# Performance work log

Measured on AMD Instinct MI355X. Metric: run time of the kernel, lower is better.

The kernel has to match this reference:

```python
import jax, jax.numpy as jnp
import numpy as np

N = 50000
E = 800000
IN_DIM = 128
HID = 64
OUT_DIM = 1
NEG_SLOPE = 0.2
EPS = 1e-16


def _glorot(key, shape):
    fan = shape[-1] + (shape[0] if len(shape) > 1 else shape[-1])
    lim = jnp.sqrt(6.0 / fan)
    return jax.random.uniform(key, shape, jnp.float32, -lim, lim)


def setup_inputs() -> dict:
    key = jax.random.key(0)
    ks = jax.random.split(key, 12)
    x = jax.random.normal(ks[0], (N, IN_DIM), jnp.float32)
    edge_index = jax.random.randint(ks[1], (2, E), 0, N, jnp.int64)
    # GATConv layer 1: in=128, out=64, heads=4, concat=True
    W1 = _glorot(ks[2], (4 * HID, IN_DIM))
    att_src1 = _glorot(ks[3], (4, HID))
    att_dst1 = _glorot(ks[4], (4, HID))
    b1 = jnp.zeros((4 * HID,), jnp.float32)
    # GATConv layer 2: in=256, out=64, heads=1, concat=True
    W2 = _glorot(ks[5], (HID, 4 * HID))
    att_src2 = _glorot(ks[6], (1, HID))
    att_dst2 = _glorot(ks[7], (1, HID))
    b2 = jnp.zeros((HID,), jnp.float32)
    # final Linear(hidden, 1)
    fc_w = _glorot(ks[8], (OUT_DIM, HID))
    fc_b = jnp.zeros((OUT_DIM,), jnp.float32)
    return {"x": x, "edge_index": edge_index, "W1": W1, "att_src1": att_src1,
            "att_dst1": att_dst1, "b1": b1, "W2": W2, "att_src2": att_src2,
            "att_dst2": att_dst2, "b2": b2, "fc_w": fc_w, "fc_b": fc_b}


def _gat_layer(x, src, dst, W, att_src, att_dst, bias, heads, out_ch):
    n = x.shape[0]
    xt = (x @ W.T).reshape(n, heads, out_ch)          # [N, H, C]
    a_src = jnp.sum(xt * att_src[None], axis=-1)      # [N, H]
    a_dst = jnp.sum(xt * att_dst[None], axis=-1)      # [N, H]
    e = a_src[src] + a_dst[dst]                       # [E', H]
    e = jnp.where(e > 0, e, NEG_SLOPE * e)            # LeakyReLU(0.2)
    # segment softmax over incoming edges of each dst node
    m = jax.ops.segment_max(e, dst, num_segments=n)
    e = jnp.exp(e - m[dst])
    s = jax.ops.segment_sum(e, dst, num_segments=n)
    alpha = e / (s[dst] + EPS)                        # [E', H]
    msg = xt[src] * alpha[:, :, None]                 # [E', H, C]
    out = jax.ops.segment_sum(msg, dst, num_segments=n)
    return out.reshape(n, heads * out_ch) + bias


def reference(x, edge_index, W1, att_src1, att_dst1, b1,
              W2, att_src2, att_dst2, b2, fc_w, fc_b):
    n = x.shape[0]
    # PyG GATConv default: add self-loops
    loops = jnp.arange(n, dtype=edge_index.dtype)
    src = jnp.concatenate([edge_index[0], loops])
    dst = jnp.concatenate([edge_index[1], loops])
    h = jax.nn.relu(_gat_layer(x, src, dst, W1, att_src1, att_dst1, b1, 4, HID))
    h = jax.nn.relu(_gat_layer(h, src, dst, W2, att_src2, att_dst2, b2, 1, HID))
    logits = h @ fc_w.T + fc_b                        # [N, 1]
    return jax.nn.sigmoid(logits).squeeze()
```

## Files before the change

### kernel.cpp

```cpp
#include <hip/hip_runtime.h>
#include <hip/hip_bf16.h>

#define NN 50000
#define EE 800000
#define ET (NN + EE)
#define SG ((NN + 255) / 256)
#define GB1 ((NN + 63) / 64)
#define GA  391
#define GBB (GB1 - GA)
#define HB  782

typedef __attribute__((ext_vector_type(8))) short short8;
typedef __attribute__((ext_vector_type(4))) short short4b;
typedef __attribute__((ext_vector_type(4))) float f32x4;

__device__ __forceinline__ float bf2f(unsigned short u) {
    union { unsigned int i; float f; } v; v.i = ((unsigned int)u) << 16; return v.f;
}
__device__ __forceinline__ unsigned short f2bf(float f) {
    __hip_bfloat16 h = __float2bfloat16(f);
    return *reinterpret_cast<unsigned short*>(&h);
}
__device__ __forceinline__ float lrelu(float e) { return fmaxf(e, 0.2f * e); }


__global__ __launch_bounds__(256) void k_scan1(const int* __restrict__ cnt,
                                               int* __restrict__ tmp, int* __restrict__ bsum) {
    int b = blockIdx.x, t = threadIdx.x, i = b * 256 + t;
    int lane = t & 63, w = t >> 6;
    int v = (i < NN) ? cnt[i] : 0;
    int s = v;
    #pragma unroll
    for (int off = 1; off < 64; off <<= 1) {
        int u = __shfl_up(s, off);
        if (lane >= off) s += u;
    }
    __shared__ int ws[4];
    if (lane == 63) ws[w] = s;
    __syncthreads();
    if (t == 0) {
        int a = 0;
        #pragma unroll
        for (int k = 0; k < 4; k++) { int x = ws[k]; ws[k] = a; a += x; }
        bsum[b] = a;
    }
    __syncthreads();
    s += ws[w];
    if (i < NN) tmp[i] = s;
}

__global__ __launch_bounds__(256) void k_scan2(const int* __restrict__ bsum, int* __restrict__ boff) {
    int t = threadIdx.x, lane = t & 63, w = t >> 6;
    int v = (t < SG) ? bsum[t] : 0;
    int s = v;
    #pragma unroll
    for (int off = 1; off < 64; off <<= 1) {
        int u = __shfl_up(s, off);
        if (lane >= off) s += u;
    }
    __shared__ int ws[4];
    if (lane == 63) ws[w] = s;
    __syncthreads();
    if (t == 0) {
        int a = 0;
        #pragma unroll
        for (int k = 0; k < 4; k++) { int x = ws[k]; ws[k] = a; a += x; }
    }
    __syncthreads();
    s += ws[w];
    if (t < SG) boff[t] = s - v;
}

__global__ void k_scan3_prep(const int* __restrict__ tmp, const int* __restrict__ boff,
                             int* __restrict__ rowptr, int* __restrict__ csr) {
    int i = blockIdx.x * blockDim.x + threadIdx.x;
    if (i == 0) rowptr[0] = 0;
    if (i < NN) {
        int base = boff[i >> 8];
        int incl = tmp[i] + base + i + 1;
        rowptr[i + 1] = incl;
        int excl = ((i & 255) ? tmp[i - 1] + base : base) + i;
        csr[excl] = i;
    }
}

template<int K, int N, int NH, bool A_BF16, bool B_BF16>
__device__ __forceinline__ void gemm_body(
    int bid, const void* __restrict__ Aptr, const void* __restrict__ Wptr,
    const float* __restrict__ atts, const float* __restrict__ attd,
    unsigned short* __restrict__ C, float* __restrict__ as_, float* __restrict__ ad_,
    int M)
{
    constexpr int KU  = K / 8;
    constexpr int KUH = KU / 2;
    constexpr int KC  = K / 32;
    constexpr int NW  = N / 4;
    constexpr int NI  = NW / 16;
    constexpr int ABYTES = 64 * KU * 16;
    constexpr int BBYTES = N * KUH * 16;
    constexpr int SMEM = ABYTES + BBYTES + (NH == 1 ? 2048 : 0);
    __shared__ char smem[SMEM];
    char* Ash = smem;
    char* Bsh = smem + ABYTES;
    unsigned short* Csh = (unsigned short*)smem;
    float* scsh = (float*)(smem + ABYTES + BBYTES);

    int t = threadIdx.x;
    int lane = t & 63, w = t >> 6;
    int colL = lane & 15, quad = lane >> 4;
    int m0 = bid * 64;

    {
        constexpr int CNT = 64 * KU / 256;
        #pragma unroll
        for (int i = 0; i < CNT; i++) {
            int v = t + 256 * i;
            int m = v / KU, u = v % KU;
            int gr = m0 + m; if (gr >= M) gr = M - 1;
            short8 val;
            if (A_BF16) {
                val = *(const short8*)((const unsigned short*)Aptr + (size_t)gr * K + u * 8);
            } else {
                const float* Af = (const float*)Aptr;
                float4 lo = *(const float4*)(Af + (size_t)gr * K + u * 8);
                float4 hi = *(const float4*)(Af + (size_t)gr * K + u * 8 + 4);
                val[0] = (short)f2bf(lo.x); val[1] = (short)f2bf(lo.y);
                val[2] = (short)f2bf(lo.z); val[3] = (short)f2bf(lo.w);
                val[4] = (short)f2bf(hi.x); val[5] = (short)f2bf(hi.y);
                val[6] = (short)f2bf(hi.z); val[7] = (short)f2bf(hi.w);
            }
            *(short8*)(Ash + ((size_t)m * KU + (u ^ (m & 7))) * 16) = val;
        }
    }

    f32x4 acc[4][NI];
    #pragma unroll
    for (int mi = 0; mi < 4; mi++)
        #pragma unroll
        for (int ni = 0; ni < NI; ni++) acc[mi][ni] = (f32x4){0.f, 0.f, 0.f, 0.f};

    #pragma unroll
    for (int kh = 0; kh < 2; kh++) {
        __syncthreads();
        {
            constexpr int CNT = N * KUH / 256;
            #pragma unroll
            for (int i = 0; i < CNT; i++) {
                int v = t + 256 * i;
                int n = v / KUH, uu = v % KUH;
                int u = kh * KUH + uu;
                short8 val;
                if (B_BF16) {
                    val = *(const short8*)((const unsigned short*)Wptr + (size_t)n * K + u * 8);
                } else {
                    const float* Wf = (const float*)Wptr;
                    float4 lo = *(const float4*)(Wf + (size_t)n * K + u * 8);
                    float4 hi = *(const float4*)(Wf + (size_t)n * K + u * 8 + 4);
                    val[0] = (short)f2bf(lo.x); val[1] = (short)f2bf(lo.y);
                    val[2] = (short)f2bf(lo.z); val[3] = (short)f2bf(lo.w);
                    val[4] = (short)f2bf(hi.x); val[5] = (short)f2bf(hi.y);
                    val[6] = (short)f2bf(hi.z); val[7] = (short)f2bf(hi.w);
                }
                *(short8*)(Bsh + ((size_t)n * KUH + (uu ^ (n & 7))) * 16) = val;
            }
        }
        __syncthreads();
        #pragma unroll
        for (int kcl = 0; kcl < KC / 2; kcl++) {
            int uA = (kh * (KC / 2) + kcl) * 4 + quad;
            int uB = kcl * 4 + quad;
            short8 bfr[NI];
            #pragma unroll
            for (int ni = 0; ni < NI; ni++) {
                int n = w * NW + ni * 16 + colL;
                bfr[ni] = *(const short8*)(Bsh + ((size_t)n * KUH + (uB ^ (n & 7))) * 16);
            }
            #pragma unroll
            for (int mi = 0; mi < 4; mi++) {
                int m = mi * 16 + colL;
                short8 af = *(const short8*)(Ash + ((size_t)m * KU + (uA ^ (m & 7))) * 16);
                #pragma unroll
                for (int ni = 0; ni < NI; ni++)
                    acc[mi][ni] = __builtin_amdgcn_mfma_f32_16x16x32_bf16(af, bfr[ni], acc[mi][ni], 0, 0, 0);
            }
        }
    }
    __syncthreads();

    float asv[NI], adv[NI];
    #pragma unroll
    for (int ni = 0; ni < NI; ni++) {
        int na = (NH == 4) ? (w * 64 + ni * 16 + colL) : (w * 16 + colL);
        asv[ni] = atts[na];
        adv[ni] = attd[na];
    }
    #pragma unroll
    for (int mi = 0; mi < 4; mi++) {
        float ps[4] = {0.f, 0.f, 0.f, 0.f}, pd[4] = {0.f, 0.f, 0.f, 0.f};
        #pragma unroll
        for (int ni = 0; ni < NI; ni++)
            #pragma unroll
            for (int r = 0; r < 4; r++) {
                ps[r] += acc[mi][ni][r] * asv[ni];
                pd[r] += acc[mi][ni][r] * adv[ni];
            }
        #pragma unroll
        for (int off = 1; off < 16; off <<= 1)
            #pragma unroll
            for (int r = 0; r < 4; r++) {
                ps[r] += __shfl_xor(ps[r], off);
                pd[r] += __shfl_xor(pd[r], off);
            }
        if (colL == 0) {
            #pragma unroll
            for (int r = 0; r < 4; r++) {
                int rloc = mi * 16 + quad * 4 + r;
                if (NH == 4) {
                    int row = m0 + rloc;
                    if (row < M) {
                        as_[(size_t)row * 4 + w] = ps[r];
                        ad_[(size_t)row * 4 + w] = pd[r];
                    }
                } else {
                    scsh[(w * 64 + rloc) * 2 + 0] = ps[r];
                    scsh[(w * 64 + rloc) * 2 + 1] = pd[r];
                }
            }
        }
    }

    #pragma unroll
    for (int mi = 0; mi < 4; mi++)
        #pragma unroll
        for (int ni = 0; ni < NI; ni++)
            #pragma unroll
            for (int r = 0; r < 4; r++)
                Csh[(size_t)(mi * 16 + quad * 4 + r) * (N + 8) + w * NW + ni * 16 + colL] =
                    f2bf(acc[mi][ni][r]);
    __syncthreads();

    {
        constexpr int CNT = 64 * (N / 8) / 256;
        #pragma unroll
        for (int i = 0; i < CNT; i++) {
            int v = t + 256 * i;
            int m = v / (N / 8), u = v % (N / 8);
            int row = m0 + m;
            if (row < M)
                *(short8*)(C + (size_t)row * N + u * 8) =
                    *(const short8*)(Csh + (size_t)m * (N + 8) + u * 8);
        }
    }
    if (NH == 1 && t < 64) {
        int row = m0 + t;
        if (row < M) {
            float s = 0.f, d = 0.f;
            #pragma unroll
            for (int ww = 0; ww < 4; ww++) {
                s += scsh[(ww * 64 + t) * 2 + 0];
                d += scsh[(ww * 64 + t) * 2 + 1];
            }
            as_[row] = s;
            ad_[row] = d;
        }
    }
}

template<int K, int N, int NH, bool A_BF16, bool B_BF16>
__global__ __launch_bounds__(256) void k_gemm_mfma(
    const void* __restrict__ Aptr, const void* __restrict__ Wptr,
    const float* __restrict__ atts, const float* __restrict__ attd,
    unsigned short* __restrict__ C, float* __restrict__ as_, float* __restrict__ ad_,
    int M)
{
    gemm_body<K, N, NH, A_BF16, B_BF16>(blockIdx.x, Aptr, Wptr, atts, attd, C, as_, ad_, M);
}

__global__ __launch_bounds__(256) void k_gemm1_hist(
    const void* __restrict__ Aptr, const void* __restrict__ Wptr,
    const float* __restrict__ atts, const float* __restrict__ attd,
    unsigned short* __restrict__ C, float* __restrict__ as_, float* __restrict__ ad_,
    int M,
    const int* __restrict__ dst, int* __restrict__ cnt, int* __restrict__ rank,
    const float* __restrict__ W2, unsigned short* __restrict__ w2b)
{
    int bid = blockIdx.x;
    bool isg; int ord;
    if (bid < 2 * GA) { isg = !(bid & 1); ord = bid >> 1; }
    else              { isg = false;      ord = bid - GA; }
    if (isg) {
        gemm_body<128, 256, 4, false, false>(ord, Aptr, Wptr, atts, attd, C, as_, ad_, M);
    } else {
        int t = threadIdx.x;
        if (ord < 16) {
            int j = ord * 256 + t;
            float4 v = *(const float4*)(W2 + j * 4);
            short4b o;
            o[0] = (short)f2bf(v.x); o[1] = (short)f2bf(v.y);
            o[2] = (short)f2bf(v.z); o[3] = (short)f2bf(v.w);
            *(short4b*)(w2b + j * 4) = o;
        }
        int i4 = ord * 256 + t;
        if (i4 < EE / 4) {
            int base = i4 * 4;
            int4 d = *(const int4*)(dst + base);
            int4 rr;
            rr.x = atomicAdd(&cnt[d.x], 1);
            rr.y = atomicAdd(&cnt[d.y], 1);
            rr.z = atomicAdd(&cnt[d.z], 1);
            rr.w = atomicAdd(&cnt[d.w], 1);
            *(int4*)(rank + base) = rr;
        }
    }
}

__global__ __launch_bounds__(256) void k_gemm1_scatter(
    const void* __restrict__ Aptr, const void* __restrict__ Wptr,
    const float* __restrict__ atts, const float* __restrict__ attd,
    unsigned short* __restrict__ C, float* __restrict__ as_, float* __restrict__ ad_,
    int M,
    const int* __restrict__ src, const int* __restrict__ dst,
    const int* __restrict__ rank, const int* __restrict__ rowptr,
    int* __restrict__ csr)
{
    int bid = blockIdx.x;
    bool isg; int ord;
    if (bid < 2 * GBB) { isg = !(bid & 1); ord = bid >> 1; }
    else               { isg = false;      ord = bid - GBB; }
    if (isg) {
        gemm_body<128, 256, 4, false, false>(GA + ord, Aptr, Wptr, atts, attd, C, as_, ad_, M);
    } else {
        int i4 = ord * 256 + threadIdx.x;
        if (i4 < EE / 4) {
            int base = i4 * 4;
            int4 d = *(const int4*)(dst + base);
            int4 r = *(const int4*)(rank + base);
            int4 s = *(const int4*)(src + base);
            csr[rowptr[d.x] + 1 + r.x] = s.x;
            csr[rowptr[d.y] + 1 + r.y] = s.y;
            csr[rowptr[d.z] + 1 + r.z] = s.z;
            csr[rowptr[d.w] + 1 + r.w] = s.w;
        }
    }
}

__global__ __launch_bounds__(256) void k_l1_agg(
    const unsigned short* __restrict__ xt1, const float* __restrict__ as1,
    const float* __restrict__ ad1, const int* __restrict__ rowptr,
    const int* __restrict__ csr, const float* __restrict__ b1,
    unsigned short* __restrict__ h1)
{
    int t = threadIdx.x;
    int lane = t & 63, w = t >> 6;
    int n = blockIdx.x * 4 + w;
    int beg = rowptr[n], deg = rowptr[n + 1] - beg;
    int half = lane >> 5, c = lane & 31, h = c >> 3;
    float adh = ad1[n * 4 + h];
    const char* xb = (const char*)xt1;
    const char* ab = (const char*)as1;
    unsigned co = (unsigned)(c << 4);
    unsigned ho = (unsigned)(h << 2);

    float acc[8] = {0.f, 0.f, 0.f, 0.f, 0.f, 0.f, 0.f, 0.f};
    float esum = 0.f;
    int j = 0;
    for (; j + 8 <= deg; j += 8) {
        int p = beg + j + half * 4;
        int s0 = csr[p], s1 = csr[p + 1], s2 = csr[p + 2], s3 = csr[p + 3];
        float a0 = *(const float*)(ab + ((unsigned)(s0 << 4) + ho));
        float a1 = *(const float*)(ab + ((unsigned)(s1 << 4) + ho));
        float a2 = *(const float*)(ab + ((unsigned)(s2 << 4) + ho));
        float a3 = *(const float*)(ab + ((unsigned)(s3 << 4) + ho));
        short8 r0 = *(const short8*)(xb + ((unsigned)(s0 << 9) + co));
        short8 r1 = *(const short8*)(xb + ((unsigned)(s1 << 9) + co));
        short8 r2 = *(const short8*)(xb + ((unsigned)(s2 << 9) + co));
        short8 r3 = *(const short8*)(xb + ((unsigned)(s3 << 9) + co));
        float e0 = __expf(lrelu(a0 + adh));
        float e1 = __expf(lrelu(a1 + adh));
        float e2 = __expf(lrelu(a2 + adh));
        float e3 = __expf(lrelu(a3 + adh));
        esum += (e0 + e1) + (e2 + e3);
        #pragma unroll
        for (int k = 0; k < 8; k++)
            acc[k] += (bf2f((unsigned short)r0[k]) * e0 + bf2f((unsigned short)r1[k]) * e1)
                    + (bf2f((unsigned short)r2[k]) * e2 + bf2f((unsigned short)r3[k]) * e3);
    }
    if (j + 4 <= deg) {
        int p = beg + j + half * 2;
        int s0 = csr[p], s1 = csr[p + 1];
        float a0 = *(const float*)(ab + ((unsigned)(s0 << 4) + ho));
        float a1 = *(const float*)(ab + ((unsigned)(s1 << 4) + ho));
        short8 r0 = *(const short8*)(xb + ((unsigned)(s0 << 9) + co));
        short8 r1 = *(const short8*)(xb + ((unsigned)(s1 << 9) + co));
        float e0 = __expf(lrelu(a0 + adh));
        float e1 = __expf(lrelu(a1 + adh));
        esum += e0 + e1;
        #pragma unroll
        for (int k = 0; k < 8; k++)
            acc[k] += bf2f((unsigned short)r0[k]) * e0 + bf2f((unsigned short)r1[k]) * e1;
        j += 4;
    }
    for (; j < deg; j += 2) {
        int jj = j + half;
        if (jj < deg) {
            int s = csr[beg + jj];
            float a0 = *(const float*)(ab + ((unsigned)(s << 4) + ho));
            short8 r = *(const short8*)(xb + ((unsigned)(s << 9) + co));
            float e = __expf(lrelu(a0 + adh));
            esum += e;
            #pragma unroll
            for (int k = 0; k < 8; k++) acc[k] += bf2f((unsigned short)r[k]) * e;
        }
    }
    #pragma unroll
    for (int k = 0; k < 8; k++) acc[k] += __shfl_xor(acc[k], 32);
    esum += __shfl_xor(esum, 32);
    if (half == 0) {
        float rs = 1.f / (esum + 1e-16f);
        float4 bl = *(const float4*)(b1 + c * 8);
        float4 bh = *(const float4*)(b1 + c * 8 + 4);
        float bb[8] = {bl.x, bl.y, bl.z, bl.w, bh.x, bh.y, bh.z, bh.w};
        short8 o;
        #pragma unroll
        for (int k = 0; k < 8; k++)
            o[k] = (short)f2bf(fmaxf(acc[k] * rs + bb[k], 0.f));
        *(short8*)(h1 + (size_t)n * 256 + c * 8) = o;
    }
}

__global__ __launch_bounds__(256) void k_l2_agg(
    const unsigned short* __restrict__ xt2, const float* __restrict__ as2,
    const float* __restrict__ ad2, const int* __restrict__ rowptr,
    const int* __restrict__ csr, const float* __restrict__ b2,
    const float* __restrict__ fcw, const float* __restrict__ fcb,
    float* __restrict__ out)
{
    int t = threadIdx.x;
    int lane = t & 63, w = t >> 6;
    int n = blockIdx.x * 4 + w;
    int beg = rowptr[n], deg = rowptr[n + 1] - beg;
    int q = lane >> 4, c = lane & 15;
    float adv = ad2[n];
    const char* xb = (const char*)xt2;
    unsigned co = (unsigned)(c << 3);

    float acc[4] = {0.f, 0.f, 0.f, 0.f};
    float esum = 0.f;
    int j = 0;
    if (deg >= 16) {
        int p = beg + q * 4;
        int s0 = csr[p], s1 = csr[p + 1], s2 = csr[p + 2], s3 = csr[p + 3];
        float a0 = as2[s0], a1 = as2[s1], a2 = as2[s2], a3 = as2[s3];
        uint2 r0 = *(const uint2*)(xb + ((unsigned)(s0 << 7) + co));
        uint2 r1 = *(const uint2*)(xb + ((unsigned)(s1 << 7) + co));
        uint2 r2 = *(const uint2*)(xb + ((unsigned)(s2 << 7) + co));
        uint2 r3 = *(const uint2*)(xb + ((unsigned)(s3 << 7) + co));
        for (; j + 32 <= deg; j += 16) {
            int p2 = beg + j + 16 + q * 4;
            int u0 = csr[p2], u1 = csr[p2 + 1], u2 = csr[p2 + 2], u3 = csr[p2 + 3];
            float f0 = as2[u0], f1 = as2[u1], f2 = as2[u2], f3 = as2[u3];
            uint2 q0 = *(const uint2*)(xb + ((unsigned)(u0 << 7) + co));
            uint2 q1 = *(const uint2*)(xb + ((unsigned)(u1 << 7) + co));
            uint2 q2 = *(const uint2*)(xb + ((unsigned)(u2 << 7) + co));
            uint2 q3 = *(const uint2*)(xb + ((unsigned)(u3 << 7) + co));
            float e0 = __expf(lrelu(a0 + adv));
            float e1 = __expf(lrelu(a1 + adv));
            float e2 = __expf(lrelu(a2 + adv));
            float e3 = __expf(lrelu(a3 + adv));
            esum += (e0 + e1) + (e2 + e3);
            acc[0] += (bf2f((unsigned short)(r0.x & 0xffff)) * e0 + bf2f((unsigned short)(r1.x & 0xffff)) * e1)
                    + (bf2f((unsigned short)(r2.x & 0xffff)) * e2 + bf2f((unsigned short)(r3.x & 0xffff)) * e3);
            acc[1] += (bf2f((unsigned short)(r0.x >> 16)) * e0 + bf2f((unsigned short)(r1.x >> 16)) * e1)
                    + (bf2f((unsigned short)(r2.x >> 16)) * e2 + bf2f((unsigned short)(r3.x >> 16)) * e3);
            acc[2] += (bf2f((unsigned short)(r0.y & 0xffff)) * e0 + bf2f((unsigned short)(r1.y & 0xffff)) * e1)
                    + (bf2f((unsigned short)(r2.y & 0xffff)) * e2 + bf2f((unsigned short)(r3.y & 0xffff)) * e3);
            acc[3] += (bf2f((unsigned short)(r0.y >> 16)) * e0 + bf2f((unsigned short)(r1.y >> 16)) * e1)
                    + (bf2f((unsigned short)(r2.y >> 16)) * e2 + bf2f((unsigned short)(r3.y >> 16)) * e3);
            a0 = f0; a1 = f1; a2 = f2; a3 = f3;
            r0 = q0; r1 = q1; r2 = q2; r3 = q3;
        }
        {
            float e0 = __expf(lrelu(a0 + adv));
            float e1 = __expf(lrelu(a1 + adv));
            float e2 = __expf(lrelu(a2 + adv));
            float e3 = __expf(lrelu(a3 + adv));
            esum += (e0 + e1) + (e2 + e3);
            acc[0] += (bf2f((unsigned short)(r0.x & 0xffff)) * e0 + bf2f((unsigned short)(r1.x & 0xffff)) * e1)
                    + (bf2f((unsigned short)(r2.x & 0xffff)) * e2 + bf2f((unsigned short)(r3.x & 0xffff)) * e3);
            acc[1] += (bf2f((unsigned short)(r0.x >> 16)) * e0 + bf2f((unsigned short)(r1.x >> 16)) * e1)
                    + (bf2f((unsigned short)(r2.x >> 16)) * e2 + bf2f((unsigned short)(r3.x >> 16)) * e3);
            acc[2] += (bf2f((unsigned short)(r0.y & 0xffff)) * e0 + bf2f((unsigned short)(r1.y & 0xffff)) * e1)
                    + (bf2f((unsigned short)(r2.y & 0xffff)) * e2 + bf2f((unsigned short)(r3.y & 0xffff)) * e3);
            acc[3] += (bf2f((unsigned short)(r0.y >> 16)) * e0 + bf2f((unsigned short)(r1.y >> 16)) * e1)
                    + (bf2f((unsigned short)(r2.y >> 16)) * e2 + bf2f((unsigned short)(r3.y >> 16)) * e3);
            j += 16;
        }
    }
    if (j + 8 <= deg) {
        int p = beg + j + q * 2;
        int s0 = csr[p], s1 = csr[p + 1];
        float a0 = as2[s0], a1 = as2[s1];
        uint2 r0 = *(const uint2*)(xb + ((unsigned)(s0 << 7) + co));
        uint2 r1 = *(const uint2*)(xb + ((unsigned)(s1 << 7) + co));
        float e0 = __expf(lrelu(a0 + adv));
        float e1 = __expf(lrelu(a1 + adv));
        esum += e0 + e1;
        acc[0] += bf2f((unsigned short)(r0.x & 0xffff)) * e0 + bf2f((unsigned short)(r1.x & 0xffff)) * e1;
        acc[1] += bf2f((unsigned short)(r0.x >> 16)) * e0 + bf2f((unsigned short)(r1.x >> 16)) * e1;
        acc[2] += bf2f((unsigned short)(r0.y & 0xffff)) * e0 + bf2f((unsigned short)(r1.y & 0xffff)) * e1;
        acc[3] += bf2f((unsigned short)(r0.y >> 16)) * e0 + bf2f((unsigned short)(r1.y >> 16)) * e1;
        j += 8;
    }
    for (; j < deg; j += 4) {
        int jj = j + q;
        if (jj < deg) {
            int s = csr[beg + jj];
            float a0 = as2[s];
            uint2 r = *(const uint2*)(xb + ((unsigned)(s << 7) + co));
            float e = __expf(lrelu(a0 + adv));
            esum += e;
            acc[0] += bf2f((unsigned short)(r.x & 0xffff)) * e;
            acc[1] += bf2f((unsigned short)(r.x >> 16)) * e;
            acc[2] += bf2f((unsigned short)(r.y & 0xffff)) * e;
            acc[3] += bf2f((unsigned short)(r.y >> 16)) * e;
        }
    }
    #pragma unroll
    for (int k = 0; k < 4; k++) {
        acc[k] += __shfl_xor(acc[k], 16);
        acc[k] += __shfl_xor(acc[k], 32);
    }
    esum += __shfl_xor(esum, 16);
    esum += __shfl_xor(esum, 32);
    float rs = 1.f / (esum + 1e-16f);
    float4 bv = *(const float4*)(b2 + c * 4);
    float4 fv = *(const float4*)(fcw + c * 4);
    float z = fmaxf(acc[0] * rs + bv.x, 0.f) * fv.x
            + fmaxf(acc[1] * rs + bv.y, 0.f) * fv.y
            + fmaxf(acc[2] * rs + bv.z, 0.f) * fv.z
            + fmaxf(acc[3] * rs + bv.w, 0.f) * fv.w;
    #pragma unroll
    for (int off = 8; off; off >>= 1) z += __shfl_xor(z, off);
    if (lane == 0) out[n] = 1.f / (1.f + __expf(-(z + fcb[0])));
}


extern "C" void kernel_launch(void* const* d_in, const int* in_sizes, int n_in,
                              void* d_out, int out_size, void* d_ws, size_t ws_size,
                              hipStream_t stream) {
    const float* x    = (const float*)d_in[0];
    const int*   ei   = (const int*)d_in[1];
    const float* W1   = (const float*)d_in[2];
    const float* as1w = (const float*)d_in[3];
    const float* ad1w = (const float*)d_in[4];
    const float* b1   = (const float*)d_in[5];
    const float* W2   = (const float*)d_in[6];
    const float* as2w = (const float*)d_in[7];
    const float* ad2w = (const float*)d_in[8];
    const float* b2   = (const float*)d_in[9];
    const float* fcw  = (const float*)d_in[10];
    const float* fcb  = (const float*)d_in[11];
    float* out = (float*)d_out;

    const int* src = ei;
    const int* dst = ei + EE;

    char* base = (char*)d_ws;
    size_t off = 0;
    auto alloc = [&](size_t bytes) -> void* {
        void* p = base + off;
        off = (off + bytes + 255) & ~(size_t)255;
        return p;
    };
    int*   rowptr   = (int*)alloc((NN + 1) * sizeof(int));
    int*   cnt      = (int*)alloc(NN * sizeof(int));
    int*   tmp      = (int*)alloc(NN * sizeof(int));
    int*   bsum     = (int*)alloc(SG * sizeof(int));
    int*   boff     = (int*)alloc(SG * sizeof(int));
    int*   rank     = (int*)alloc(EE * sizeof(int));
    int*   csr      = (int*)alloc(ET * sizeof(int));
    unsigned short* xt1 = (unsigned short*)alloc((size_t)NN * 256 * sizeof(unsigned short));
    unsigned short* h1  = (unsigned short*)alloc((size_t)NN * 256 * sizeof(unsigned short));
    unsigned short* w2b = (unsigned short*)alloc(64 * 256 * sizeof(unsigned short));
    float* as1      = (float*)alloc(NN * 4 * sizeof(float));
    float* ad1      = (float*)alloc(NN * 4 * sizeof(float));
    float* as2      = (float*)alloc(NN * sizeof(float));
    float* ad2      = (float*)alloc(NN * sizeof(float));
    unsigned short* xt2 = xt1;

    hipMemsetAsync(cnt, 0, NN * sizeof(int), stream);

    k_gemm1_hist<<<2 * GA + (HB - GA), 256, 0, stream>>>(
        x, W1, as1w, ad1w, xt1, as1, ad1, NN, dst, cnt, rank, W2, w2b);

    k_scan1<<<SG, 256, 0, stream>>>(cnt, tmp, bsum);
    k_scan2<<<1, 256, 0, stream>>>(bsum, boff);
    k_scan3_prep<<<SG, 256, 0, stream>>>(tmp, boff, rowptr, csr);

    k_gemm1_scatter<<<2 * GBB + (HB - GBB), 256, 0, stream>>>(
        x, W1, as1w, ad1w, xt1, as1, ad1, NN, src, dst, rank, rowptr, csr);

    k_l1_agg<<<(NN + 3) / 4, 256, 0, stream>>>(xt1, as1, ad1, rowptr, csr, b1, h1);
    k_gemm_mfma<256, 64, 1, true, true><<<GB1, 256, 0, stream>>>(
        h1, w2b, as2w, ad2w, xt2, as2, ad2, NN);
    k_l2_agg<<<(NN + 3) / 4, 256, 0, stream>>>(xt2, as2, ad2, rowptr, csr, b2, fcw, fcb, out);
}
```

Before: 267.0 us.

## Fuse three-kernel scan into decoupled look-back scan; widen layer-2 aggregation loads

Replaces the three-pass prefix scan (block scan, block-sum scan, fixup) with a single-pass decoupled look-back scan. Each block publishes its aggregate or inclusive prefix through flagged atomics and spins on its predecessors. This saves two kernel launches and the intermediate tmp/boff round-trips. Separately, the layer-2 aggregation now has each lane load 16-byte rows covering 8 channels instead of 8-byte rows covering 4, with 8 edge groups per wavefront instead of 4. That adds one more shuffle reduction stage and relies on forward progress of earlier blocks for the spin-wait.

```diff
diff --git a/kernel.cpp b/kernel.cpp
--- a/kernel.cpp
+++ b/kernel.cpp
@@ -23,9 +23,10 @@
 }
 __device__ __forceinline__ float lrelu(float e) { return fmaxf(e, 0.2f * e); }
 
-
-__global__ __launch_bounds__(256) void k_scan1(const int* __restrict__ cnt,
-                                               int* __restrict__ tmp, int* __restrict__ bsum) {
+__global__ __launch_bounds__(256) void k_scan_fused(
+    const int* __restrict__ cnt, int* __restrict__ st,
+    int* __restrict__ rowptr, int* __restrict__ csr)
+{
     int b = blockIdx.x, t = threadIdx.x, i = b * 256 + t;
     int lane = t & 63, w = t >> 6;
     int v = (i < NN) ? cnt[i] : 0;
@@ -36,50 +37,54 @@
         if (lane >= off) s += u;
     }
     __shared__ int ws[4];
+    __shared__ int exsh;
     if (lane == 63) ws[w] = s;
     __syncthreads();
+    int a = 0;
     if (t == 0) {
-        int a = 0;
         #pragma unroll
         for (int k = 0; k < 4; k++) { int x = ws[k]; ws[k] = a; a += x; }
-        bsum[b] = a;
+        int flag = (b == 0) ? 2 : 1;
+        __hip_atomic_store(&st[b], (a << 2) | flag, __ATOMIC_RELEASE, __HIP_MEMORY_SCOPE_AGENT);
+    }
+    if (w == 0 && b > 0) {
+        int ex = 0;
+        int base = b - 1;
+        for (;;) {
+            int idx = base - lane;
+            int pv = 0;
+            if (idx >= 0) {
+                do {
+                    pv = __hip_atomic_load(&st[idx], __ATOMIC_ACQUIRE, __HIP_MEMORY_SCOPE_AGENT);
+                } while ((pv & 3) == 0);
+            }
+            bool incl = (idx >= 0) && ((pv & 3) == 2);
+            unsigned long long m = __ballot(incl);
+            int contrib;
+            if (m) {
+                int fi = __ffsll((long long)m) - 1;
+                contrib = (idx >= 0 && lane <= fi) ? (pv >> 2) : 0;
+            } else {
+                contrib = (idx >= 0) ? (pv >> 2) : 0;
+            }
+            #pragma unroll
+            for (int off = 1; off < 64; off <<= 1) contrib += __shfl_xor(contrib, off);
+            ex += contrib;
+            if (m) break;
+            base -= 64;
+        }
+        if (lane == 0) {
+            __hip_atomic_store(&st[b], ((a + ex) << 2) | 2, __ATOMIC_RELEASE, __HIP_MEMORY_SCOPE_AGENT);
+            exsh = ex;
+        }
     }
     __syncthreads();
-    s += ws[w];
-    if (i < NN) tmp[i] = s;
-}
-
-__global__ __launch_bounds__(256) void k_scan2(const int* __restrict__ bsum, int* __restrict__ boff) {
-    int t = threadIdx.x, lane = t & 63, w = t >> 6;
-    int v = (t < SG) ? bsum[t] : 0;
-    int s = v;
-    #pragma unroll
-    for (int off = 1; off < 64; off <<= 1) {
-        int u = __shfl_up(s, off);
-        if (lane >= off) s += u;
-    }
-    __shared__ int ws[4];
-    if (lane == 63) ws[w] = s;
-    __syncthreads();
-    if (t == 0) {
-        int a = 0;
-        #pragma unroll
-        for (int k = 0; k < 4; k++) { int x = ws[k]; ws[k] = a; a += x; }
-    }
-    __syncthreads();
-    s += ws[w];
-    if (t < SG) boff[t] = s - v;
-}
-
-__global__ void k_scan3_prep(const int* __restrict__ tmp, const int* __restrict__ boff,
-                             int* __restrict__ rowptr, int* __restrict__ csr) {
-    int i = blockIdx.x * blockDim.x + threadIdx.x;
+    s += ws[w] + ((b > 0) ? exsh : 0);
     if (i == 0) rowptr[0] = 0;
     if (i < NN) {
-        int base = boff[i >> 8];
-        int incl = tmp[i] + base + i + 1;
+        int incl = s + i + 1;
         rowptr[i + 1] = incl;
-        int excl = ((i & 255) ? tmp[i - 1] + base : base) + i;
+        int excl = incl - v - 1;
         csr[excl] = i;
     }
 }
@@ -439,108 +444,113 @@
     int lane = t & 63, w = t >> 6;
     int n = blockIdx.x * 4 + w;
     int beg = rowptr[n], deg = rowptr[n + 1] - beg;
-    int q = lane >> 4, c = lane & 15;
+    int o = lane >> 3, c = lane & 7;
     float adv = ad2[n];
     const char* xb = (const char*)xt2;
-    unsigned co = (unsigned)(c << 3);
-
-    float acc[4] = {0.f, 0.f, 0.f, 0.f};
+    unsigned co = (unsigned)(c << 4);
+
+    float acc[8] = {0.f, 0.f, 0.f, 0.f, 0.f, 0.f, 0.f, 0.f};
     float esum = 0.f;
     int j = 0;
     if (deg >= 16) {
-        int p = beg + q * 4;
-        int s0 = csr[p], s1 = csr[p + 1], s2 = csr[p + 2], s3 = csr[p + 3];
-        float a0 = as2[s0], a1 = as2[s1], a2 = as2[s2], a3 = as2[s3];
-        uint2 r0 = *(const uint2*)(xb + ((unsigned)(s0 << 7) + co));
-        uint2 r1 = *(const uint2*)(xb + ((unsigned)(s1 << 7) + co));
-        uint2 r2 = *(const uint2*)(xb + ((unsigned)(s2 << 7) + co));
-        uint2 r3 = *(const uint2*)(xb + ((unsigned)(s3 << 7) + co));
+        int p = beg + o * 2;
+        int s0 = csr[p], s1 = csr[p + 1];
+        float a0 = as2[s0], a1 = as2[s1];
+        uint4 r0 = *(const uint4*)(xb + ((unsigned)(s0 << 7) + co));
+        uint4 r1 = *(const uint4*)(xb + ((unsigned)(s1 << 7) + co));
         for (; j + 32 <= deg; j += 16) {
-            int p2 = beg + j + 16 + q * 4;
-            int u0 = csr[p2], u1 = csr[p2 + 1], u2 = csr[p2 + 2], u3 = csr[p2 + 3];
-            float f0 = as2[u0], f1 = as2[u1], f2 = as2[u2], f3 = as2[u3];
-            uint2 q0 = *(const uint2*)(xb + ((unsigned)(u0 << 7) + co));
-            uint2 q1 = *(const uint2*)(xb + ((unsigned)(u1 << 7) + co));
-            uint2 q2 = *(const uint2*)(xb + ((unsigned)(u2 << 7) + co));
-            uint2 q3 = *(const uint2*)(xb + ((unsigned)(u3 << 7) + co));
+            int p2 = beg + j + 16 + o * 2;
+            int u0 = csr[p2], u1 = csr[p2 + 1];
+            float f0 = as2[u0], f1 = as2[u1];
+            uint4 q0 = *(const uint4*)(xb + ((unsigned)(u0 << 7) + co));
+            uint4 q1 = *(const uint4*)(xb + ((unsigned)(u1 << 7) + co));
             float e0 = __expf(lrelu(a0 + adv));
             float e1 = __expf(lrelu(a1 + adv));
-            float e2 = __expf(lrelu(a2 + adv));
-            float e3 = __expf(lrelu(a3 + adv));
-            esum += (e0 + e1) + (e2 + e3);
-            acc[0] += (bf2f((unsigned short)(r0.x & 0xffff)) * e0 + bf2f((unsigned short)(r1.x & 0xffff)) * e1)
-                    + (bf2f((unsigned short)(r2.x & 0xffff)) * e2 + bf2f((unsigned short)(r3.x & 0xffff)) * e3);
-            acc[1] += (bf2f((unsigned short)(r0.x >> 16)) * e0 + bf2f((unsigned short)(r1.x >> 16)) * e1)
-                    + (bf2f((unsigned short)(r2.x >> 16)) * e2 + bf2f((unsigned short)(r3.x >> 16)) * e3);
-            acc[2] += (bf2f((unsigned short)(r0.y & 0xffff)) * e0 + bf2f((unsigned short)(r1.y & 0xffff)) * e1)
-                    + (bf2f((unsigned short)(r2.y & 0xffff)) * e2 + bf2f((unsigned short)(r3.y & 0xffff)) * e3);
-            acc[3] += (bf2f((unsigned short)(r0.y >> 16)) * e0 + bf2f((unsigned short)(r1.y >> 16)) * e1)
-                    + (bf2f((unsigned short)(r2.y >> 16)) * e2 + bf2f((unsigned short)(r3.y >> 16)) * e3);
-            a0 = f0; a1 = f1; a2 = f2; a3 = f3;
-            r0 = q0; r1 = q1; r2 = q2; r3 = q3;
+            esum += e0 + e1;
+            acc[0] += bf2f((unsigned short)(r0.x & 0xffff)) * e0 + bf2f((unsigned short)(r1.x & 0xffff)) * e1;
+            acc[1] += bf2f((unsigned short)(r0.x >> 16))   * e0 + bf2f((unsigned short)(r1.x >> 16))   * e1;
+            acc[2] += bf2f((unsigned short)(r0.y & 0xffff)) * e0 + bf2f((unsigned short)(r1.y & 0xffff)) * e1;
+            acc[3] += bf2f((unsigned short)(r0.y >> 16))   * e0 + bf2f((unsigned short)(r1.y >> 16))   * e1;
+            acc[4] += bf2f((unsigned short)(r0.z & 0xffff)) * e0 + bf2f((unsigned short)(r1.z & 0xffff)) * e1;
+            acc[5] += bf2f((unsigned short)(r0.z >> 16))   * e0 + bf2f((unsigned short)(r1.z >> 16))   * e1;
+            acc[6] += bf2f((unsigned short)(r0.w & 0xffff)) * e0 + bf2f((unsigned short)(r1.w & 0xffff)) * e1;
+            acc[7] += bf2f((unsigned short)(r0.w >> 16))   * e0 + bf2f((unsigned short)(r1.w >> 16))   * e1;
+            a0 = f0; a1 = f1; r0 = q0; r1 = q1;
         }
         {
             float e0 = __expf(lrelu(a0 + adv));
             float e1 = __expf(lrelu(a1 + adv));
-            float e2 = __expf(lrelu(a2 + adv));
-            float e3 = __expf(lrelu(a3 + adv));
-            esum += (e0 + e1) + (e2 + e3);
-            acc[0] += (bf2f((unsigned short)(r0.x & 0xffff)) * e0 + bf2f((unsigned short)(r1.x & 0xffff)) * e1)
-                    + (bf2f((unsigned short)(r2.x & 0xffff)) * e2 + bf2f((unsigned short)(r3.x & 0xffff)) * e3);
-            acc[1] += (bf2f((unsigned short)(r0.x >> 16)) * e0 + bf2f((unsigned short)(r1.x >> 16)) * e1)
-                    + (bf2f((unsigned short)(r2.x >> 16)) * e2 + bf2f((unsigned short)(r3.x >> 16)) * e3);
-            acc[2] += (bf2f((unsigned short)(r0.y & 0xffff)) * e0 + bf2f((unsigned short)(r1.y & 0xffff)) * e1)
-                    + (bf2f((unsigned short)(r2.y & 0xffff)) * e2 + bf2f((unsigned short)(r3.y & 0xffff)) * e3);
-            acc[3] += (bf2f((unsigned short)(r0.y >> 16)) * e0 + bf2f((unsigned short)(r1.y >> 16)) * e1)
-                    + (bf2f((unsigned short)(r2.y >> 16)) * e2 + bf2f((unsigned short)(r3.y >> 16)) * e3);
+            esum += e0 + e1;
+            acc[0] += bf2f((unsigned short)(r0.x & 0xffff)) * e0 + bf2f((unsigned short)(r1.x & 0xffff)) * e1;
+            acc[1] += bf2f((unsigned short)(r0.x >> 16))   * e0 + bf2f((unsigned short)(r1.x >> 16))   * e1;
+            acc[2] += bf2f((unsigned short)(r0.y & 0xffff)) * e0 + bf2f((unsigned short)(r1.y & 0xffff)) * e1;
+            acc[3] += bf2f((unsigned short)(r0.y >> 16))   * e0 + bf2f((unsigned short)(r1.y >> 16))   * e1;
+            acc[4] += bf2f((unsigned short)(r0.z & 0xffff)) * e0 + bf2f((unsigned short)(r1.z & 0xffff)) * e1;
+            acc[5] += bf2f((unsigned short)(r0.z >> 16))   * e0 + bf2f((unsigned short)(r1.z >> 16))   * e1;
+            acc[6] += bf2f((unsigned short)(r0.w & 0xffff)) * e0 + bf2f((unsigned short)(r1.w & 0xffff)) * e1;
+            acc[7] += bf2f((unsigned short)(r0.w >> 16))   * e0 + bf2f((unsigned short)(r1.w >> 16))   * e1;
             j += 16;
         }
     }
     if (j + 8 <= deg) {
-        int p = beg + j + q * 2;
-        int s0 = csr[p], s1 = csr[p + 1];
-        float a0 = as2[s0], a1 = as2[s1];
-        uint2 r0 = *(const uint2*)(xb + ((unsigned)(s0 << 7) + co));
-        uint2 r1 = *(const uint2*)(xb + ((unsigned)(s1 << 7) + co));
+        int s0 = csr[beg + j + o];
+        float a0 = as2[s0];
+        uint4 r0 = *(const uint4*)(xb + ((unsigned)(s0 << 7) + co));
         float e0 = __expf(lrelu(a0 + adv));
-        float e1 = __expf(lrelu(a1 + adv));
-        esum += e0 + e1;
-        acc[0] += bf2f((unsigned short)(r0.x & 0xffff)) * e0 + bf2f((unsigned short)(r1.x & 0xffff)) * e1;
-        acc[1] += bf2f((unsigned short)(r0.x >> 16)) * e0 + bf2f((unsigned short)(r1.x >> 16)) * e1;
-        acc[2] += bf2f((unsigned short)(r0.y & 0xffff)) * e0 + bf2f((unsigned short)(r1.y & 0xffff)) * e1;
-        acc[3] += bf2f((unsigned short)(r0.y >> 16)) * e0 + bf2f((unsigned short)(r1.y >> 16)) * e1;
+        esum += e0;
+        acc[0] += bf2f((unsigned short)(r0.x & 0xffff)) * e0;
+        acc[1] += bf2f((unsigned short)(r0.x >> 16))   * e0;
+        acc[2] += bf2f((unsigned short)(r0.y & 0xffff)) * e0;
+        acc[3] += bf2f((unsigned short)(r0.y >> 16))   * e0;
+        acc[4] += bf2f((unsigned short)(r0.z & 0xffff)) * e0;
+        acc[5] += bf2f((unsigned short)(r0.z >> 16))   * e0;
+        acc[6] += bf2f((unsigned short)(r0.w & 0xffff)) * e0;
+        acc[7] += bf2f((unsigned short)(r0.w >> 16))   * e0;
         j += 8;
     }
-    for (; j < deg; j += 4) {
-        int jj = j + q;
+    {
+        int jj = j + o;
         if (jj < deg) {
-            int s = csr[beg + jj];
-            float a0 = as2[s];
-            uint2 r = *(const uint2*)(xb + ((unsigned)(s << 7) + co));
-            float e = __expf(lrelu(a0 + adv));
-            esum += e;
-            acc[0] += bf2f((unsigned short)(r.x & 0xffff)) * e;
-            acc[1] += bf2f((unsigned short)(r.x >> 16)) * e;
-            acc[2] += bf2f((unsigned short)(r.y & 0xffff)) * e;
-            acc[3] += bf2f((unsigned short)(r.y >> 16)) * e;
-        }
-    }
-    #pragma unroll
-    for (int k = 0; k < 4; k++) {
+            int s0 = csr[beg + jj];
+            float a0 = as2[s0];
+            uint4 r0 = *(const uint4*)(xb + ((unsigned)(s0 << 7) + co));
+            float e0 = __expf(lrelu(a0 + adv));
+            esum += e0;
+            acc[0] += bf2f((unsigned short)(r0.x & 0xffff)) * e0;
+            acc[1] += bf2f((unsigned short)(r0.x >> 16))   * e0;
+            acc[2] += bf2f((unsigned short)(r0.y & 0xffff)) * e0;
+            acc[3] += bf2f((unsigned short)(r0.y >> 16))   * e0;
+            acc[4] += bf2f((unsigned short)(r0.z & 0xffff)) * e0;
+            acc[5] += bf2f((unsigned short)(r0.z >> 16))   * e0;
+            acc[6] += bf2f((unsigned short)(r0.w & 0xffff)) * e0;
+            acc[7] += bf2f((unsigned short)(r0.w >> 16))   * e0;
+        }
+    }
+    #pragma unroll
+    for (int k = 0; k < 8; k++) {
+        acc[k] += __shfl_xor(acc[k], 8);
         acc[k] += __shfl_xor(acc[k], 16);
         acc[k] += __shfl_xor(acc[k], 32);
     }
+    esum += __shfl_xor(esum, 8);
     esum += __shfl_xor(esum, 16);
     esum += __shfl_xor(esum, 32);
     float rs = 1.f / (esum + 1e-16f);
-    float4 bv = *(const float4*)(b2 + c * 4);
-    float4 fv = *(const float4*)(fcw + c * 4);
-    float z = fmaxf(acc[0] * rs + bv.x, 0.f) * fv.x
-            + fmaxf(acc[1] * rs + bv.y, 0.f) * fv.y
-            + fmaxf(acc[2] * rs + bv.z, 0.f) * fv.z
-            + fmaxf(acc[3] * rs + bv.w, 0.f) * fv.w;
-    #pragma unroll
-    for (int off = 8; off; off >>= 1) z += __shfl_xor(z, off);
+    float4 b0 = *(const float4*)(b2 + c * 8);
+    float4 b1v = *(const float4*)(b2 + c * 8 + 4);
+    float4 f0v = *(const float4*)(fcw + c * 8);
+    float4 f1v = *(const float4*)(fcw + c * 8 + 4);
+    float z = fmaxf(acc[0] * rs + b0.x, 0.f) * f0v.x
+            + fmaxf(acc[1] * rs + b0.y, 0.f) * f0v.y
+            + fmaxf(acc[2] * rs + b0.z, 0.f) * f0v.z
+            + fmaxf(acc[3] * rs + b0.w, 0.f) * f0v.w
+            + fmaxf(acc[4] * rs + b1v.x, 0.f) * f1v.x
+            + fmaxf(acc[5] * rs + b1v.y, 0.f) * f1v.y
+            + fmaxf(acc[6] * rs + b1v.z, 0.f) * f1v.z
+            + fmaxf(acc[7] * rs + b1v.w, 0.f) * f1v.w;
+    z += __shfl_xor(z, 1);
+    z += __shfl_xor(z, 2);
+    z += __shfl_xor(z, 4);
     if (lane == 0) out[n] = 1.f / (1.f + __expf(-(z + fcb[0])));
 }
 
@@ -573,10 +583,8 @@
         return p;
     };
     int*   rowptr   = (int*)alloc((NN + 1) * sizeof(int));
-    int*   cnt      = (int*)alloc(NN * sizeof(int));
-    int*   tmp      = (int*)alloc(NN * sizeof(int));
-    int*   bsum     = (int*)alloc(SG * sizeof(int));
-    int*   boff     = (int*)alloc(SG * sizeof(int));
+    int*   cnt      = (int*)alloc((NN + SG) * sizeof(int));
+    int*   st       = cnt + NN;
     int*   rank     = (int*)alloc(EE * sizeof(int));
     int*   csr      = (int*)alloc(ET * sizeof(int));
     unsigned short* xt1 = (unsigned short*)alloc((size_t)NN * 256 * sizeof(unsigned short));
@@ -588,14 +596,12 @@
     float* ad2      = (float*)alloc(NN * sizeof(float));
     unsigned short* xt2 = xt1;
 
-    hipMemsetAsync(cnt, 0, NN * sizeof(int), stream);
+    hipMemsetAsync(cnt, 0, (NN + SG) * sizeof(int), stream);
 
     k_gemm1_hist<<<2 * GA + (HB - GA), 256, 0, stream>>>(
         x, W1, as1w, ad1w, xt1, as1, ad1, NN, dst, cnt, rank, W2, w2b);
 
-    k_scan1<<<SG, 256, 0, stream>>>(cnt, tmp, bsum);
-    k_scan2<<<1, 256, 0, stream>>>(bsum, boff);
-    k_scan3_prep<<<SG, 256, 0, stream>>>(tmp, boff, rowptr, csr);
+    k_scan_fused<<<SG, 256, 0, stream>>>(cnt, st, rowptr, csr);
 
     k_gemm1_scatter<<<2 * GBB + (HB - GBB), 256, 0, stream>>>(
         x, W1, as1w, ad1w, xt1, as1, ad1, NN, src, dst, rank, rowptr, csr);
```

Result: slower. 276.1 us (+3.4%).
